# Performance work log

Hardware: AMD Instinct MI355X
Metric: run time of the kernel (lower is better)

The kernel has to match this reference:

```python
import jax, jax.numpy as jnp
import numpy as np

# --- boolean gate helpers on {0,1}-valued float pulses ---
def OR(a, b):
    return a + b - a * b

def AND(a, b):
    return a * b

def NOT(a):
    return 1.0 - a

def XOR(a, b):
    return a + b - 2.0 * a * b

def MUX(sel, a, b):
    # sel ? a : b (broadcasts sel over last dim)
    return sel * a + (1.0 - sel) * b


def setup_inputs() -> dict:
    key = jax.random.key(0)
    shape = (8192, 2048, 8)
    fp8_pulse = (jax.random.uniform(key, shape) < 0.5).astype(jnp.float32)
    return {"fp8_pulse": fp8_pulse}


def reference(fp8_pulse):
    batch_shape = fp8_pulse.shape[:-1]
    dt = fp8_pulse.dtype
    zeros = jnp.zeros(batch_shape + (1,), dtype=dt)
    ones = jnp.ones(batch_shape + (1,), dtype=dt)

    s  = fp8_pulse[..., 0:1]
    e3 = fp8_pulse[..., 1:2]
    e2 = fp8_pulse[..., 2:3]
    e1 = fp8_pulse[..., 3:4]
    e0 = fp8_pulse[..., 4:5]
    m2 = fp8_pulse[..., 5:6]
    m1 = fp8_pulse[..., 6:7]
    m0 = fp8_pulse[..., 7:8]

    e_nonzero = OR(OR(e0, e1), OR(e2, e3))
    e_is_zero = NOT(e_nonzero)
    m_nonzero = OR(OR(m0, m1), m2)
    is_subnormal = AND(e_is_zero, m_nonzero)

    # 5-bit ripple-carry adder (LSB-first): fp8_exp + 8
    a_bits = [e0, e1, e2, e3, zeros]
    b_bits = [zeros, zeros, zeros, ones, zeros]  # const 8, LSB-first
    carry = zeros
    sum_bits = []
    for i in range(5):
        axb = XOR(a_bits[i], b_bits[i])
        sum_bits.append(XOR(axb, carry))
        carry = OR(AND(a_bits[i], b_bits[i]), AND(carry, axb))
    # MSB-first FP16 exponent for the normal case
    fp16_exp_normal = jnp.concatenate(sum_bits[::-1], axis=-1)

    fp16_mant_normal = jnp.concatenate([m2, m1, m0] + [zeros] * 7, axis=-1)

    # leading-one detection for subnormal FP8
    lead_at_2 = m2
    lead_at_1 = AND(NOT(m2), m1)
    lead_at_0 = AND(AND(NOT(m2), NOT(m1)), m0)
    _ = lead_at_1  # kept for faithfulness; not used downstream (as in original)

    exp_8 = jnp.concatenate([zeros, ones, zeros, zeros, zeros], axis=-1)
    exp_7 = jnp.concatenate([zeros, zeros, ones, ones, ones], axis=-1)
    exp_6 = jnp.concatenate([zeros, zeros, ones, ones, zeros], axis=-1)

    sub_exp_01 = MUX(lead_at_0, exp_6, exp_7)
    sub_exp = MUX(lead_at_2, exp_8, sub_exp_01)

    mant_lead2 = jnp.concatenate([m1, m0] + [zeros] * 8, axis=-1)
    mant_lead1 = jnp.concatenate([m0] + [zeros] * 9, axis=-1)
    mant_lead0 = jnp.concatenate([zeros] * 10, axis=-1)

    sub_mant_01 = MUX(lead_at_0, mant_lead0, mant_lead1)
    sub_mant = MUX(lead_at_2, mant_lead2, sub_mant_01)

    is_zero = AND(e_is_zero, NOT(m_nonzero))
    not_is_zero = NOT(is_zero)

    fp16_exp = AND(MUX(is_subnormal, sub_exp, fp16_exp_normal), not_is_zero)
    fp16_mant = AND(MUX(is_subnormal, sub_mant, fp16_mant_normal), not_is_zero)

    return jnp.concatenate([s, fp16_exp, fp16_mant], axis=-1)
```

## Files before the change

### kernel.cpp

```cpp
#include <hip/hip_runtime.h>
#include <cstdint>


__global__ __launch_bounds__(256) void fp8_to_fp16_bits_kernel(
    const float4* __restrict__ in4,
    float4* __restrict__ out4,
    int n_groups)
{
    int idx = blockIdx.x * blockDim.x + threadIdx.x;
    int stride = gridDim.x * blockDim.x;
    for (int g = idx; g < n_groups; g += stride) {
        float4 a = in4[2 * g];
        float4 b = in4[2 * g + 1];

        uint32_t s  = a.x != 0.0f;
        uint32_t e3 = a.y != 0.0f;
        uint32_t e2 = a.z != 0.0f;
        uint32_t e1 = a.w != 0.0f;
        uint32_t e0 = b.x != 0.0f;
        uint32_t m2 = b.y != 0.0f;
        uint32_t m1 = b.z != 0.0f;
        uint32_t m0 = b.w != 0.0f;

        uint32_t e = (e3 << 3) | (e2 << 2) | (e1 << 1) | e0;
        uint32_t m = (m2 << 2) | (m1 << 1) | m0;

        uint32_t exp5, mant10;
        if (e) {
            exp5 = e + 8u;
            mant10 = m << 7;
        } else if (m2) {
            exp5 = 8u;
            mant10 = (m & 3u) << 8;
        } else if (m1) {
            exp5 = 7u;
            mant10 = (m & 1u) << 9;
        } else if (m0) {
            exp5 = 6u;
            mant10 = 0u;
        } else {
            exp5 = 0u;
            mant10 = 0u;
        }

        uint32_t word = (s << 15) | (exp5 << 10) | mant10;

        float o[16];
        #pragma unroll
        for (int j = 0; j < 16; ++j)
            o[j] = (float)((word >> (15 - j)) & 1u);

        float4* op = out4 + 4 * g;
        op[0] = make_float4(o[0],  o[1],  o[2],  o[3]);
        op[1] = make_float4(o[4],  o[5],  o[6],  o[7]);
        op[2] = make_float4(o[8],  o[9],  o[10], o[11]);
        op[3] = make_float4(o[12], o[13], o[14], o[15]);
    }
}

extern "C" void kernel_launch(void* const* d_in, const int* in_sizes, int n_in,
                              void* d_out, int out_size, void* d_ws, size_t ws_size,
                              hipStream_t stream)
{
    const float4* in4 = (const float4*)d_in[0];
    float4* out4 = (float4*)d_out;
    int n_groups = in_sizes[0] / 8;

    dim3 grid(2048), block(256);
    fp8_to_fp16_bits_kernel<<<grid, block, 0, stream>>>(in4, out4, n_groups);
}
```

Before: 1.586 ms.

## Map one thread per output float4 for coalesced stores

```diff
diff --git a/kernel.cpp b/kernel.cpp
--- a/kernel.cpp
+++ b/kernel.cpp
@@ -5,11 +5,13 @@
 __global__ __launch_bounds__(256) void fp8_to_fp16_bits_kernel(
     const float4* __restrict__ in4,
     float4* __restrict__ out4,
-    int n_groups)
+    int n_out4)
 {
     int idx = blockIdx.x * blockDim.x + threadIdx.x;
     int stride = gridDim.x * blockDim.x;
-    for (int g = idx; g < n_groups; g += stride) {
+    for (int o = idx; o < n_out4; o += stride) {
+        int g = o >> 2;
+        int q = o & 3;
         float4 a = in4[2 * g];
         float4 b = in4[2 * g + 1];
 
@@ -25,36 +27,26 @@
         uint32_t e = (e3 << 3) | (e2 << 2) | (e1 << 1) | e0;
         uint32_t m = (m2 << 2) | (m1 << 1) | m0;
 
-        uint32_t exp5, mant10;
-        if (e) {
-            exp5 = e + 8u;
-            mant10 = m << 7;
-        } else if (m2) {
-            exp5 = 8u;
-            mant10 = (m & 3u) << 8;
-        } else if (m1) {
-            exp5 = 7u;
-            mant10 = (m & 1u) << 9;
-        } else if (m0) {
-            exp5 = 6u;
-            mant10 = 0u;
-        } else {
-            exp5 = 0u;
-            mant10 = 0u;
-        }
+        uint32_t exp5  = e  ? e + 8u
+                       : m2 ? 8u
+                       : m1 ? 7u
+                       : m0 ? 6u
+                       :      0u;
+        uint32_t mant10 = e  ? (m << 7)
+                        : m2 ? ((m & 3u) << 8)
+                        : m1 ? ((m & 1u) << 9)
+                        :      0u;
 
         uint32_t word = (s << 15) | (exp5 << 10) | mant10;
 
-        float o[16];
-        #pragma unroll
-        for (int j = 0; j < 16; ++j)
-            o[j] = (float)((word >> (15 - j)) & 1u);
+        int sh = 15 - 4 * q;
+        float4 r;
+        r.x = ((word >> (sh    )) & 1u) ? 1.0f : 0.0f;
+        r.y = ((word >> (sh - 1)) & 1u) ? 1.0f : 0.0f;
+        r.z = ((word >> (sh - 2)) & 1u) ? 1.0f : 0.0f;
+        r.w = ((word >> (sh - 3)) & 1u) ? 1.0f : 0.0f;
 
-        float4* op = out4 + 4 * g;
-        op[0] = make_float4(o[0],  o[1],  o[2],  o[3]);
-        op[1] = make_float4(o[4],  o[5],  o[6],  o[7]);
-        op[2] = make_float4(o[8],  o[9],  o[10], o[11]);
-        op[3] = make_float4(o[12], o[13], o[14], o[15]);
+        out4[o] = r;
     }
 }
 
@@ -64,8 +56,8 @@
 {
     const float4* in4 = (const float4*)d_in[0];
     float4* out4 = (float4*)d_out;
-    int n_groups = in_sizes[0] / 8;
+    int n_out4 = out_size / 4;
 
     dim3 grid(2048), block(256);
-    fp8_to_fp16_bits_kernel<<<grid, block, 0, stream>>>(in4, out4, n_groups);
+    fp8_to_fp16_bits_kernel<<<grid, block, 0, stream>>>(in4, out4, n_out4);
 }
```

After: 1.366 ms. -13.8%, faster.
